# Optimization experiments

Measured on AMD Instinct MI355X. Metric: run time of the kernel, lower is better.

The kernel has to match this reference:

```python
import jax, jax.numpy as jnp
import numpy as np

H = 16  # num_attention_heads


def setup_inputs() -> dict:
    key = jax.random.key(0)
    k1, k2, k3 = jax.random.split(key, 3)
    B, S, E = 2, 2048, 1024
    return {
        "hidden_states": jax.random.normal(k1, (B, S, E), dtype=jnp.float32),
        "W_attn": jax.random.normal(k2, (E, 3 * E), dtype=jnp.float32) * 0.02,
        "b_attn": jnp.zeros((3 * E,), dtype=jnp.float32),
        "W_proj": jax.random.normal(k3, (E, E), dtype=jnp.float32) * 0.02,
        "b_proj": jnp.zeros((E,), dtype=jnp.float32),
    }


def reference(hidden_states, W_attn, b_attn, W_proj, b_proj):
    B, S, E = hidden_states.shape
    hd = E // H
    # Conv1D: x @ W + b -> [B, S, 3E]
    qkv = hidden_states @ W_attn + b_attn
    # Faithful to module: _split_heads with 3*head_dim FIRST, then split q/k/v.
    # i.e. per-head slice of size 3*hd is [q_h | k_h | v_h] (interleaved layout).
    qkv = qkv.reshape(B, S, H, 3 * hd).transpose(0, 2, 1, 3)  # [B, H, S, 3*hd]
    q, k, v = jnp.split(qkv, 3, axis=-1)                      # each [B, H, S, hd]
    # scores, scaled by sqrt(head_dim) (value.size(-1) ** 0.5)
    scores = jnp.einsum("bhqd,bhkd->bhqk", q, k) / jnp.asarray(hd, q.dtype) ** 0.5
    # causal mask via where with masked_bias = -10000.0 (not -inf), as in module
    causal = jnp.tril(jnp.ones((S, S), dtype=bool))
    scores = jnp.where(causal, scores, jnp.asarray(-10000.0, scores.dtype))
    attn_weights = jax.nn.softmax(scores, axis=-1)  # dropout p=0 -> identity
    attn_out = jnp.einsum("bhqk,bhkd->bhqd", attn_weights, v)
    attn_out = attn_out.transpose(0, 2, 1, 3).reshape(B, S, E)  # merge heads
    return attn_out @ W_proj + b_proj
```

## Files before the change

kernel.cpp:

```cpp
#include <hip/hip_runtime.h>
#include <hip/hip_bf16.h>


typedef __attribute__((ext_vector_type(4))) float f32x4;
typedef __attribute__((ext_vector_type(16))) float f32x16;
typedef __attribute__((ext_vector_type(8))) short short8;
typedef __attribute__((ext_vector_type(2))) unsigned int uint2v;

#define AS1 __attribute__((address_space(1)))
#define AS3 __attribute__((address_space(3)))

__device__ __forceinline__ void load_lds16(const void* g, void* l) {
    __builtin_amdgcn_global_load_lds((const AS1 void*)g, (AS3 void*)l, 16, 0, 0);
}

__device__ __forceinline__ unsigned short f2bf(float f) {
    union { float f; unsigned int u; } v; v.f = f;
    unsigned int r = v.u + 0x7FFFu + ((v.u >> 16) & 1u);
    return (unsigned short)(r >> 16);
}

__device__ __forceinline__ int cvt_pk_bf16(float lo, float hi) {
    int r;
    asm("v_cvt_pk_bf16_f32 %0, %1, %2" : "=v"(r) : "v"(lo), "v"(hi));
    return r;
}

__device__ __forceinline__ void transpose_tile(
    const float* __restrict__ W, unsigned short* __restrict__ Wt,
    int K, int N, int bx, int by, int t) {
    __shared__ float tile[32][33];
    int k0 = by * 32, n0 = bx * 32;
    int r = t >> 3, c = (t & 7) * 4;
    float4 v = *(const float4*)&W[(size_t)(k0 + r) * N + n0 + c];
    tile[r][c] = v.x; tile[r][c + 1] = v.y; tile[r][c + 2] = v.z; tile[r][c + 3] = v.w;
    __syncthreads();
    int n = t >> 3; int kk = (t & 7) * 4;
    ushort4 o;
    o.x = f2bf(tile[kk + 0][n]);
    o.y = f2bf(tile[kk + 1][n]);
    o.z = f2bf(tile[kk + 2][n]);
    o.w = f2bf(tile[kk + 3][n]);
    *(ushort4*)&Wt[(size_t)(n0 + n) * K + k0 + kk] = o;
}

__global__ __launch_bounds__(256) void prep(
    const float* __restrict__ hs, unsigned short* __restrict__ Xb,
    const float* __restrict__ W_attn, unsigned short* __restrict__ WaT,
    const float* __restrict__ W_proj, unsigned short* __restrict__ WpT) {
    int bid = blockIdx.x, t = threadIdx.x;
    if (bid < 4096) {
        int i = (bid * 256 + t) * 4;
        float4 v = *(const float4*)(hs + i);
        ushort4 o;
        o.x = f2bf(v.x); o.y = f2bf(v.y); o.z = f2bf(v.z); o.w = f2bf(v.w);
        *(ushort4*)(Xb + i) = o;
    } else if (bid < 7168) {
        int r = bid - 4096;
        transpose_tile(W_attn, WaT, 1024, 3072, r % 96, r / 96, t);
    } else {
        int r = bid - 7168;
        transpose_tile(W_proj, WpT, 1024, 1024, r % 32, r / 32, t);
    }
}

__global__ __launch_bounds__(256) void gemm_qkv(
    const unsigned short* __restrict__ A,
    const unsigned short* __restrict__ Bt,
    const float* __restrict__ bias,
    unsigned short* __restrict__ qk, unsigned short* __restrict__ Vt,
    int M, int N, int K) {
    __shared__ unsigned short Sh[2][8192];
    unsigned short* Tb = &Sh[0][0];
    const int t = threadIdx.x, wave = t >> 6, lane = t & 63;
    const int l15 = lane & 15, quad = lane >> 4;
    const int m0 = blockIdx.y * 128, n0 = blockIdx.x * 128;
    const int srow = wave * 32 + (lane >> 2);
    const int sch = (lane & 3) * 8;
    const unsigned short* Ag = A + (size_t)(m0 + srow) * K + sch;
    const unsigned short* Bg = Bt + (size_t)(n0 + srow) * K + sch;
    const int wOff = wave * 1024;
    const int wm = (wave >> 1) * 64, wn = (wave & 1) * 64;
    f32x4 acc[4][4] = {};
    const int NSTEP = K / 32;
    load_lds16(Ag, &Sh[0][wOff]);
    load_lds16(Ag + (size_t)16 * K, &Sh[0][wOff + 512]);
    load_lds16(Bg, &Sh[0][4096 + wOff]);
    load_lds16(Bg + (size_t)16 * K, &Sh[0][4096 + wOff + 512]);
    for (int kt = 0; kt < NSTEP; ++kt) {
        const int cur = kt & 1;
        const unsigned short* As = &Sh[cur][0];
        const unsigned short* Bs = &Sh[cur][4096];
        __syncthreads();
        if (kt + 1 < NSTEP) {
            const int k1 = (kt + 1) * 32;
            unsigned short* An = &Sh[cur ^ 1][0];
            unsigned short* Bn = &Sh[cur ^ 1][4096];
            load_lds16(Ag + k1, An + wOff);
            load_lds16(Ag + k1 + (size_t)16 * K, An + wOff + 512);
            load_lds16(Bg + k1, Bn + wOff);
            load_lds16(Bg + k1 + (size_t)16 * K, Bn + wOff + 512);
        }
        short8 af[4], bf[4];
#pragma unroll
        for (int i = 0; i < 4; ++i) {
            af[i] = *(const short8*)&As[(wm + i * 16 + l15) * 32 + quad * 8];
            bf[i] = *(const short8*)&Bs[(wn + i * 16 + l15) * 32 + quad * 8];
        }
        __builtin_amdgcn_s_setprio(1);
#pragma unroll
        for (int mt = 0; mt < 4; ++mt)
#pragma unroll
            for (int nt = 0; nt < 4; ++nt)
                acc[mt][nt] = __builtin_amdgcn_mfma_f32_16x16x32_bf16(af[mt], bf[nt], acc[mt][nt], 0, 0, 0);
        __builtin_amdgcn_s_setprio(0);
    }
    __syncthreads();
    const int rem = n0 % 192;
#pragma unroll
    for (int mt = 0; mt < 4; ++mt) {
        int mrow = m0 + wm + mt * 16 + quad * 4;
#pragma unroll
        for (int nt = 0; nt < 4; ++nt) {
            int col = n0 + wn + nt * 16 + l15;
            float bv = bias[col];
            int h = col / 192;
            int j = col - h * 192;
            if (j < 128) {
                float sc = (j < 64) ? 0.125f : 1.0f;
#pragma unroll
                for (int r = 0; r < 4; ++r)
                    qk[(size_t)(mrow + r) * 2048 + h * 128 + j] = f2bf((acc[mt][nt][r] + bv) * sc);
            } else {
                int d = j - 128;
                int s_local = wm + mt * 16 + quad * 4;
                ushort4 pk;
                pk.x = f2bf(acc[mt][nt][0] + bv);
                pk.y = f2bf(acc[mt][nt][1] + bv);
                pk.z = f2bf(acc[mt][nt][2] + bv);
                pk.w = f2bf(acc[mt][nt][3] + bv);
                *(ushort4*)&Tb[d * 136 + s_local] = pk;
            }
        }
    }
    if (rem != 0) {
        __syncthreads();
        int vhalf = (rem == 64) ? 1 : 0;
        int h = (n0 + vhalf * 64) / 192;
        int b = m0 >> 11;
        unsigned short* vbase = Vt + ((size_t)(b * 16 + h) * 64) * 2048 + (m0 & 2047);
        int drow = t >> 4, ch = (t & 15) * 8;
#pragma unroll
        for (int rr = 0; rr < 4; ++rr) {
            int d = rr * 16 + drow;
            *(uint4*)(vbase + (size_t)d * 2048 + ch) = *(const uint4*)&Tb[d * 136 + ch];
        }
    }
}

__global__ __launch_bounds__(256) void gemm_proj(
    const unsigned short* __restrict__ A,
    const unsigned short* __restrict__ Bt,
    const float* __restrict__ bias,
    float* __restrict__ C, int M, int N, int K) {
    __shared__ unsigned short Sh[2][6144];
    const int t = threadIdx.x, wave = t >> 6, lane = t & 63;
    const int l15 = lane & 15, quad = lane >> 4;
    const int m0 = blockIdx.y * 128, n0 = blockIdx.x * 64;
    const int srowA = wave * 32 + (lane >> 2);
    const int sch = (lane & 3) * 8;
    const unsigned short* Ag = A + (size_t)(m0 + srowA) * K + sch;
    const unsigned short* Bg = Bt + (size_t)(n0 + wave * 16 + (lane >> 2)) * K + sch;
    const int aOff = wave * 1024, bOff = wave * 512;
    const int wm = (wave >> 1) * 64, wn = (wave & 1) * 32;
    f32x4 acc[4][2] = {};
    const int NSTEP = K / 32;
    load_lds16(Ag, &Sh[0][aOff]);
    load_lds16(Ag + (size_t)16 * K, &Sh[0][aOff + 512]);
    load_lds16(Bg, &Sh[0][4096 + bOff]);
    for (int kt = 0; kt < NSTEP; ++kt) {
        const int cur = kt & 1;
        const unsigned short* As = &Sh[cur][0];
        const unsigned short* Bs = &Sh[cur][4096];
        __syncthreads();
        if (kt + 1 < NSTEP) {
            const int k1 = (kt + 1) * 32;
            load_lds16(Ag + k1, &Sh[cur ^ 1][aOff]);
            load_lds16(Ag + k1 + (size_t)16 * K, &Sh[cur ^ 1][aOff + 512]);
            load_lds16(Bg + k1, &Sh[cur ^ 1][4096 + bOff]);
        }
        short8 af[4], bf[2];
#pragma unroll
        for (int i = 0; i < 4; ++i)
            af[i] = *(const short8*)&As[(wm + i * 16 + l15) * 32 + quad * 8];
#pragma unroll
        for (int i = 0; i < 2; ++i)
            bf[i] = *(const short8*)&Bs[(wn + i * 16 + l15) * 32 + quad * 8];
        __builtin_amdgcn_s_setprio(1);
#pragma unroll
        for (int mt = 0; mt < 4; ++mt)
#pragma unroll
            for (int nt = 0; nt < 2; ++nt)
                acc[mt][nt] = __builtin_amdgcn_mfma_f32_16x16x32_bf16(af[mt], bf[nt], acc[mt][nt], 0, 0, 0);
        __builtin_amdgcn_s_setprio(0);
    }
#pragma unroll
    for (int mt = 0; mt < 4; ++mt) {
        int mrow = m0 + wm + mt * 16 + quad * 4;
#pragma unroll
        for (int nt = 0; nt < 2; ++nt) {
            int col = n0 + wn + nt * 16 + l15;
            float bv = bias[col];
#pragma unroll
            for (int r = 0; r < 4; ++r)
                C[(size_t)(mrow + r) * N + col] = acc[mt][nt][r] + bv;
        }
    }
}

__global__ __launch_bounds__(256) void attn4(
    const unsigned short* __restrict__ qk,
    const unsigned short* __restrict__ Vt,
    unsigned short* __restrict__ out) {
    const int S = 2048;
    __shared__ unsigned short Ks[2][4096];
    __shared__ unsigned short Vts[2][4096];
    const int t = threadIdx.x, wave = t >> 6, lane = t & 63;
    const int l31 = lane & 31, half = lane >> 5;
    const int bid = blockIdx.x;
    const int qt = (bid < 256) ? (15 - (bid >> 5)) : ((bid - 256) >> 5);
    const int bh = bid & 31;
    const int b = bh >> 4, h = bh & 15;
    const unsigned short* qkb = qk + (size_t)b * S * 2048 + h * 128;
    const unsigned short* vtb = Vt + (size_t)bh * 64 * 2048;

    const int q0 = qt * 128 + wave * 32;
    short8 qf[4];
#pragma unroll
    for (int km = 0; km < 4; ++km)
        qf[km] = *(const short8*)(qkb + (size_t)(q0 + l31) * 2048 + km * 16 + half * 8);

    f32x16 o[2] = {};
    float lrun = 0.f;

    const int srow = t >> 2;
    const int c16a = (t & 3) * 2, c16b = c16a + 1;
    const int swzA = srow * 64 + ((c16a ^ (srow & 7)) * 8);
    const int swzB = srow * 64 + ((c16b ^ (srow & 7)) * 8);
    const int KT = qt * 2 + 2;

    uint4 kr0 = *(const uint4*)(qkb + (size_t)srow * 2048 + 64 + c16a * 8);
    uint4 kr1 = *(const uint4*)(qkb + (size_t)srow * 2048 + 64 + c16b * 8);
    uint4 vr0 = *(const uint4*)(vtb + (size_t)srow * 2048 + c16a * 8);
    uint4 vr1 = *(const uint4*)(vtb + (size_t)srow * 2048 + c16b * 8);

    const int qmax = q0 + 31;
    const int ksw = l31 & 7;
    int chs[4];
#pragma unroll
    for (int km = 0; km < 4; ++km)
        chs[km] = ((km * 2 + half) ^ ksw) * 8;
    const int krow = l31 * 64;

    for (int kt = 0; kt < KT; ++kt) {
        const int cur = kt & 1;
        *(uint4*)&Ks[cur][swzA] = kr0;
        *(uint4*)&Ks[cur][swzB] = kr1;
        *(uint4*)&Vts[cur][swzA] = vr0;
        *(uint4*)&Vts[cur][swzB] = vr1;
        __syncthreads();
        if (kt + 1 < KT) {
            const int kn = (kt + 1) * 64;
            kr0 = *(const uint4*)(qkb + (size_t)(kn + srow) * 2048 + 64 + c16a * 8);
            kr1 = *(const uint4*)(qkb + (size_t)(kn + srow) * 2048 + 64 + c16b * 8);
            vr0 = *(const uint4*)(vtb + (size_t)srow * 2048 + kn + c16a * 8);
            vr1 = *(const uint4*)(vtb + (size_t)srow * 2048 + kn + c16b * 8);
        }
        const int kb = kt * 64;
        if (kb > qmax) continue;

        f32x16 s[2] = {};
        __builtin_amdgcn_s_setprio(1);
#pragma unroll
        for (int nt = 0; nt < 2; ++nt)
#pragma unroll
            for (int km = 0; km < 4; ++km) {
                short8 kf = *(const short8*)&Ks[cur][nt * 2048 + krow + chs[km]];
                s[nt] = __builtin_amdgcn_mfma_f32_32x32x16_bf16(kf, qf[km], s[nt], 0, 0, 0);
            }
        __builtin_amdgcn_s_setprio(0);

        if (kb + 63 > q0) {
#pragma unroll
            for (int nt = 0; nt < 2; ++nt)
#pragma unroll
                for (int r = 0; r < 16; ++r) {
                    int kg = kb + nt * 32 + (r & 3) + 8 * (r >> 2) + 4 * half;
                    if (kg > q0 + l31) s[nt][r] = -1e30f;
                }
        }

        int gd[2][4][2];
        float a0 = 0.f;
#pragma unroll
        for (int nt = 0; nt < 2; ++nt)
#pragma unroll
            for (int g = 0; g < 4; ++g) {
                float e0 = __expf(s[nt][4 * g + 0]);
                float e1 = __expf(s[nt][4 * g + 1]);
                float e2 = __expf(s[nt][4 * g + 2]);
                float e3 = __expf(s[nt][4 * g + 3]);
                a0 += (e0 + e1) + (e2 + e3);
                gd[nt][g][0] = cvt_pk_bf16(e0, e1);
                gd[nt][g][1] = cvt_pk_bf16(e2, e3);
            }
        lrun += a0;

        short8 paf[4];
#pragma unroll
        for (int km = 0; km < 4; ++km) {
            const int nt = km >> 1, m = km & 1;
            uint2v w0 = __builtin_amdgcn_permlane32_swap(
                (unsigned)gd[nt][2 * m][0], (unsigned)gd[nt][2 * m + 1][0], false, false);
            uint2v w1 = __builtin_amdgcn_permlane32_swap(
                (unsigned)gd[nt][2 * m][1], (unsigned)gd[nt][2 * m + 1][1], false, false);
            int4 v = {(int)w0[0], (int)w1[0], (int)w0[1], (int)w1[1]};
            paf[km] = __builtin_bit_cast(short8, v);
        }

        __builtin_amdgcn_s_setprio(1);
#pragma unroll
        for (int nt2 = 0; nt2 < 2; ++nt2)
#pragma unroll
            for (int km = 0; km < 4; ++km) {
                short8 vf = *(const short8*)&Vts[cur][nt2 * 2048 + krow + chs[km]];
                o[nt2] = __builtin_amdgcn_mfma_f32_32x32x16_bf16(paf[km], vf, o[nt2], 0, 0, 0);
            }
        __builtin_amdgcn_s_setprio(0);
    }

    float tot = lrun + __shfl_xor(lrun, 32);
    unsigned short* ob = out + (size_t)b * S * 1024 + h * 64;
#pragma unroll
    for (int r = 0; r < 16; ++r) {
        int ql = (r & 3) + 8 * (r >> 2) + 4 * half;
        float inv = 1.0f / __shfl(tot, ql);
        size_t row = (size_t)(q0 + ql) * 1024;
        ob[row + l31] = f2bf(o[0][r] * inv);
        ob[row + 32 + l31] = f2bf(o[1][r] * inv);
    }
}

extern "C" void kernel_launch(void* const* d_in, const int* in_sizes, int n_in,
                              void* d_out, int out_size, void* d_ws, size_t ws_size,
                              hipStream_t stream) {
    const float* hs     = (const float*)d_in[0];
    const float* W_attn = (const float*)d_in[1];
    const float* b_attn = (const float*)d_in[2];
    const float* W_proj = (const float*)d_in[3];
    const float* b_proj = (const float*)d_in[4];
    float* out = (float*)d_out;

    const int B = 2, S = 2048, E = 1024;
    const int M = B * S;
    const int N3 = 3 * E;

    unsigned short* Xb  = (unsigned short*)d_ws;
    unsigned short* WaT = Xb + (size_t)M * E;
    unsigned short* WpT = WaT + (size_t)N3 * E;
    unsigned short* qkb = WpT + (size_t)E * E;
    unsigned short* Vt  = qkb + (size_t)M * 2048;
    unsigned short* ao  = Vt + (size_t)M * E;

    prep<<<dim3(8192), 256, 0, stream>>>(hs, Xb, W_attn, WaT, W_proj, WpT);

    gemm_qkv<<<dim3(N3 / 128, M / 128), 256, 0, stream>>>(Xb, WaT, b_attn, qkb, Vt, M, N3, E);

    attn4<<<dim3(512), 256, 0, stream>>>(qkb, Vt, ao);

    gemm_proj<<<dim3(E / 64, M / 128), 256, 0, stream>>>(ao, WpT, b_proj, out, M, E, E);
}
```

Baseline: 175.1 us.

## Split attention KV loop across two wave groups and fold log2e into Q scale

The attention kernel now launches 512 threads per block, with two groups of four waves. Each group handles alternate 64-key tiles, staged together into a single shared buffer per iteration, and the partial outputs and row sums are reduced through LDS at the end. Q scaling now folds in log2(e) so the softmax can use the raw v_exp_f32 (exp2) instruction instead of __expf. This doubles the parallelism per block on the sequential key loop, at the cost of an extra barrier per iteration, the loss of LDS double buffering, and a final LDS reduction.

```diff
diff --git a/kernel.cpp b/kernel.cpp
--- a/kernel.cpp
+++ b/kernel.cpp
@@ -23,6 +23,12 @@
 __device__ __forceinline__ int cvt_pk_bf16(float lo, float hi) {
     int r;
     asm("v_cvt_pk_bf16_f32 %0, %1, %2" : "=v"(r) : "v"(lo), "v"(hi));
+    return r;
+}
+
+__device__ __forceinline__ float fexp2(float x) {
+    float r;
+    asm("v_exp_f32 %0, %1" : "=v"(r) : "v"(x));
     return r;
 }
 
@@ -127,7 +133,7 @@
             int h = col / 192;
             int j = col - h * 192;
             if (j < 128) {
-                float sc = (j < 64) ? 0.125f : 1.0f;
+                float sc = (j < 64) ? 0.18033688011f : 1.0f;
 #pragma unroll
                 for (int r = 0; r < 4; ++r)
                     qk[(size_t)(mrow + r) * 2048 + h * 128 + j] = f2bf((acc[mt][nt][r] + bv) * sc);
@@ -218,15 +224,15 @@
     }
 }
 
-__global__ __launch_bounds__(256) void attn4(
+__global__ __launch_bounds__(512, 4) void attn5(
     const unsigned short* __restrict__ qk,
     const unsigned short* __restrict__ Vt,
     unsigned short* __restrict__ out) {
     const int S = 2048;
-    __shared__ unsigned short Ks[2][4096];
-    __shared__ unsigned short Vts[2][4096];
+    __shared__ unsigned short Sh[16384];
     const int t = threadIdx.x, wave = t >> 6, lane = t & 63;
     const int l31 = lane & 31, half = lane >> 5;
+    const int g = wave >> 2, gw = wave & 3;
     const int bid = blockIdx.x;
     const int qt = (bid < 256) ? (15 - (bid >> 5)) : ((bid - 256) >> 5);
     const int bh = bid & 31;
@@ -234,7 +240,7 @@
     const unsigned short* qkb = qk + (size_t)b * S * 2048 + h * 128;
     const unsigned short* vtb = Vt + (size_t)bh * 64 * 2048;
 
-    const int q0 = qt * 128 + wave * 32;
+    const int q0 = qt * 128 + gw * 32;
     short8 qf[4];
 #pragma unroll
     for (int km = 0; km < 4; ++km)
@@ -243,16 +249,14 @@
     f32x16 o[2] = {};
     float lrun = 0.f;
 
-    const int srow = t >> 2;
-    const int c16a = (t & 3) * 2, c16b = c16a + 1;
-    const int swzA = srow * 64 + ((c16a ^ (srow & 7)) * 8);
-    const int swzB = srow * 64 + ((c16b ^ (srow & 7)) * 8);
-    const int KT = qt * 2 + 2;
-
-    uint4 kr0 = *(const uint4*)(qkb + (size_t)srow * 2048 + 64 + c16a * 8);
-    uint4 kr1 = *(const uint4*)(qkb + (size_t)srow * 2048 + 64 + c16b * 8);
-    uint4 vr0 = *(const uint4*)(vtb + (size_t)srow * 2048 + c16a * 8);
-    uint4 vr1 = *(const uint4*)(vtb + (size_t)srow * 2048 + c16b * 8);
+    const int srow = t >> 3, ch16 = t & 7;
+    const int swz = srow * 64 + ((ch16 ^ (srow & 7)) * 8);
+    const int KTP = qt + 1;
+
+    uint4 kE = *(const uint4*)(qkb + (size_t)srow * 2048 + 64 + ch16 * 8);
+    uint4 kO = *(const uint4*)(qkb + (size_t)(64 + srow) * 2048 + 64 + ch16 * 8);
+    uint4 vE = *(const uint4*)(vtb + (size_t)srow * 2048 + ch16 * 8);
+    uint4 vO = *(const uint4*)(vtb + (size_t)srow * 2048 + 64 + ch16 * 8);
 
     const int qmax = q0 + 31;
     const int ksw = l31 & 7;
@@ -261,93 +265,123 @@
     for (int km = 0; km < 4; ++km)
         chs[km] = ((km * 2 + half) ^ ksw) * 8;
     const int krow = l31 * 64;
-
-    for (int kt = 0; kt < KT; ++kt) {
-        const int cur = kt & 1;
-        *(uint4*)&Ks[cur][swzA] = kr0;
-        *(uint4*)&Ks[cur][swzB] = kr1;
-        *(uint4*)&Vts[cur][swzA] = vr0;
-        *(uint4*)&Vts[cur][swzB] = vr1;
+    const unsigned short* Ksg = Sh + (g ? 4096 : 0);
+    const unsigned short* Vsg = Sh + 8192 + (g ? 4096 : 0);
+
+    for (int p = 0; p < KTP; ++p) {
+        *(uint4*)&Sh[swz] = kE;
+        *(uint4*)&Sh[4096 + swz] = kO;
+        *(uint4*)&Sh[8192 + swz] = vE;
+        *(uint4*)&Sh[12288 + swz] = vO;
         __syncthreads();
-        if (kt + 1 < KT) {
-            const int kn = (kt + 1) * 64;
-            kr0 = *(const uint4*)(qkb + (size_t)(kn + srow) * 2048 + 64 + c16a * 8);
-            kr1 = *(const uint4*)(qkb + (size_t)(kn + srow) * 2048 + 64 + c16b * 8);
-            vr0 = *(const uint4*)(vtb + (size_t)srow * 2048 + kn + c16a * 8);
-            vr1 = *(const uint4*)(vtb + (size_t)srow * 2048 + kn + c16b * 8);
-        }
-        const int kb = kt * 64;
-        if (kb > qmax) continue;
-
-        f32x16 s[2] = {};
-        __builtin_amdgcn_s_setprio(1);
-#pragma unroll
-        for (int nt = 0; nt < 2; ++nt)
+        if (p + 1 < KTP) {
+            const int k2 = (2 * p + 2) * 64, k3 = k2 + 64;
+            kE = *(const uint4*)(qkb + (size_t)(k2 + srow) * 2048 + 64 + ch16 * 8);
+            kO = *(const uint4*)(qkb + (size_t)(k3 + srow) * 2048 + 64 + ch16 * 8);
+            vE = *(const uint4*)(vtb + (size_t)srow * 2048 + k2 + ch16 * 8);
+            vO = *(const uint4*)(vtb + (size_t)srow * 2048 + k3 + ch16 * 8);
+        }
+        const int kb = (2 * p + g) * 64;
+        if (kb <= qmax) {
+            f32x16 s[2] = {};
+            __builtin_amdgcn_s_setprio(1);
+#pragma unroll
+            for (int nt = 0; nt < 2; ++nt)
+#pragma unroll
+                for (int km = 0; km < 4; ++km) {
+                    short8 kf = *(const short8*)&Ksg[nt * 2048 + krow + chs[km]];
+                    s[nt] = __builtin_amdgcn_mfma_f32_32x32x16_bf16(kf, qf[km], s[nt], 0, 0, 0);
+                }
+            __builtin_amdgcn_s_setprio(0);
+
+            if (kb + 63 > q0) {
+#pragma unroll
+                for (int nt = 0; nt < 2; ++nt)
+#pragma unroll
+                    for (int r = 0; r < 16; ++r) {
+                        int kg = kb + nt * 32 + (r & 3) + 8 * (r >> 2) + 4 * half;
+                        if (kg > q0 + l31) s[nt][r] = -1e30f;
+                    }
+            }
+
+            int gd[2][4][2];
+            float a0 = 0.f;
+#pragma unroll
+            for (int nt = 0; nt < 2; ++nt)
+#pragma unroll
+                for (int gg = 0; gg < 4; ++gg) {
+                    float e0 = fexp2(s[nt][4 * gg + 0]);
+                    float e1 = fexp2(s[nt][4 * gg + 1]);
+                    float e2 = fexp2(s[nt][4 * gg + 2]);
+                    float e3 = fexp2(s[nt][4 * gg + 3]);
+                    a0 += (e0 + e1) + (e2 + e3);
+                    gd[nt][gg][0] = cvt_pk_bf16(e0, e1);
+                    gd[nt][gg][1] = cvt_pk_bf16(e2, e3);
+                }
+            lrun += a0;
+
+            short8 paf[4];
 #pragma unroll
             for (int km = 0; km < 4; ++km) {
-                short8 kf = *(const short8*)&Ks[cur][nt * 2048 + krow + chs[km]];
-                s[nt] = __builtin_amdgcn_mfma_f32_32x32x16_bf16(kf, qf[km], s[nt], 0, 0, 0);
+                const int nt = km >> 1, m = km & 1;
+                uint2v w0 = __builtin_amdgcn_permlane32_swap(
+                    (unsigned)gd[nt][2 * m][0], (unsigned)gd[nt][2 * m + 1][0], false, false);
+                uint2v w1 = __builtin_amdgcn_permlane32_swap(
+                    (unsigned)gd[nt][2 * m][1], (unsigned)gd[nt][2 * m + 1][1], false, false);
+                int4 v = {(int)w0[0], (int)w1[0], (int)w0[1], (int)w1[1]};
+                paf[km] = __builtin_bit_cast(short8, v);
             }
-        __builtin_amdgcn_s_setprio(0);
-
-        if (kb + 63 > q0) {
-#pragma unroll
-            for (int nt = 0; nt < 2; ++nt)
-#pragma unroll
-                for (int r = 0; r < 16; ++r) {
-                    int kg = kb + nt * 32 + (r & 3) + 8 * (r >> 2) + 4 * half;
-                    if (kg > q0 + l31) s[nt][r] = -1e30f;
+
+            __builtin_amdgcn_s_setprio(1);
+#pragma unroll
+            for (int nt2 = 0; nt2 < 2; ++nt2)
+#pragma unroll
+                for (int km = 0; km < 4; ++km) {
+                    short8 vf = *(const short8*)&Vsg[nt2 * 2048 + krow + chs[km]];
+                    o[nt2] = __builtin_amdgcn_mfma_f32_32x32x16_bf16(paf[km], vf, o[nt2], 0, 0, 0);
                 }
-        }
-
-        int gd[2][4][2];
-        float a0 = 0.f;
-#pragma unroll
-        for (int nt = 0; nt < 2; ++nt)
-#pragma unroll
-            for (int g = 0; g < 4; ++g) {
-                float e0 = __expf(s[nt][4 * g + 0]);
-                float e1 = __expf(s[nt][4 * g + 1]);
-                float e2 = __expf(s[nt][4 * g + 2]);
-                float e3 = __expf(s[nt][4 * g + 3]);
-                a0 += (e0 + e1) + (e2 + e3);
-                gd[nt][g][0] = cvt_pk_bf16(e0, e1);
-                gd[nt][g][1] = cvt_pk_bf16(e2, e3);
-            }
-        lrun += a0;
-
-        short8 paf[4];
-#pragma unroll
-        for (int km = 0; km < 4; ++km) {
-            const int nt = km >> 1, m = km & 1;
-            uint2v w0 = __builtin_amdgcn_permlane32_swap(
-                (unsigned)gd[nt][2 * m][0], (unsigned)gd[nt][2 * m + 1][0], false, false);
-            uint2v w1 = __builtin_amdgcn_permlane32_swap(
-                (unsigned)gd[nt][2 * m][1], (unsigned)gd[nt][2 * m + 1][1], false, false);
-            int4 v = {(int)w0[0], (int)w1[0], (int)w0[1], (int)w1[1]};
-            paf[km] = __builtin_bit_cast(short8, v);
-        }
-
-        __builtin_amdgcn_s_setprio(1);
-#pragma unroll
-        for (int nt2 = 0; nt2 < 2; ++nt2)
-#pragma unroll
-            for (int km = 0; km < 4; ++km) {
-                short8 vf = *(const short8*)&Vts[cur][nt2 * 2048 + krow + chs[km]];
-                o[nt2] = __builtin_amdgcn_mfma_f32_32x32x16_bf16(paf[km], vf, o[nt2], 0, 0, 0);
-            }
-        __builtin_amdgcn_s_setprio(0);
-    }
-
-    float tot = lrun + __shfl_xor(lrun, 32);
-    unsigned short* ob = out + (size_t)b * S * 1024 + h * 64;
-#pragma unroll
-    for (int r = 0; r < 16; ++r) {
-        int ql = (r & 3) + 8 * (r >> 2) + 4 * half;
-        float inv = 1.0f / __shfl(tot, ql);
-        size_t row = (size_t)(q0 + ql) * 1024;
-        ob[row + l31] = f2bf(o[0][r] * inv);
-        ob[row + 32 + l31] = f2bf(o[1][r] * inv);
+            __builtin_amdgcn_s_setprio(0);
+        }
+        __syncthreads();
+    }
+
+    float* Lf = (float*)Sh;
+    const int cidx = gw * 64 + lane;
+    if (g == 1) {
+        float* dst = Lf + cidx * 17;
+#pragma unroll
+        for (int r = 0; r < 16; ++r) dst[r] = o[0][r];
+        dst[16] = lrun;
+    }
+    __syncthreads();
+    float lsum = lrun;
+    if (g == 0) {
+        const float* src = Lf + cidx * 17;
+#pragma unroll
+        for (int r = 0; r < 16; ++r) o[0][r] += src[r];
+        lsum += src[16];
+    }
+    __syncthreads();
+    if (g == 1) {
+        float* dst = Lf + cidx * 16;
+#pragma unroll
+        for (int r = 0; r < 16; ++r) dst[r] = o[1][r];
+    }
+    __syncthreads();
+    if (g == 0) {
+        const float* src = Lf + cidx * 16;
+#pragma unroll
+        for (int r = 0; r < 16; ++r) o[1][r] += src[r];
+        float tot = lsum + __shfl_xor(lsum, 32);
+        unsigned short* ob = out + (size_t)b * S * 1024 + h * 64;
+#pragma unroll
+        for (int r = 0; r < 16; ++r) {
+            int ql = (r & 3) + 8 * (r >> 2) + 4 * half;
+            float inv = 1.0f / __shfl(tot, ql);
+            size_t row = (size_t)(q0 + ql) * 1024;
+            ob[row + l31] = f2bf(o[0][r] * inv);
+            ob[row + 32 + l31] = f2bf(o[1][r] * inv);
+        }
     }
 }
 
@@ -376,7 +410,7 @@
 
     gemm_qkv<<<dim3(N3 / 128, M / 128), 256, 0, stream>>>(Xb, WaT, b_attn, qkb, Vt, M, N3, E);
 
-    attn4<<<dim3(512), 256, 0, stream>>>(qkb, Vt, ao);
+    attn5<<<dim3(512), 512, 0, stream>>>(qkb, Vt, ao);
 
     gemm_proj<<<dim3(E / 64, M / 128), 256, 0, stream>>>(ao, WpT, b_proj, out, M, E, E);
 }
```

Result: faster. 168.1 us (-4.0%).
